# Performance work log

Measured on AMD Instinct MI355X. Metric: run time of the kernel, lower is better.

Reference implementation:

```python
import jax, jax.numpy as jnp
import numpy as np

BIN_ALPHA = 1.0  # alpha mixture factor from init
NEG_SLOPE = 0.1  # LeakyReLU slope


def setup_inputs() -> dict:
    key = jax.random.key(0)
    ks = jax.random.split(key, 10)
    B, N, BIN, D = 8, 19264, 100, 768
    gene_expression = jax.random.uniform(ks[0], (B, N), dtype=jnp.float32) * 10.0
    pad_mask = jax.random.randint(ks[1], (B, N), 0, 2, dtype=jnp.int32)
    masked_mask = jax.random.randint(ks[2], (B, N), 0, 2, dtype=jnp.int32)
    # layer1: Linear(1, BIN) -> weight (BIN,1) stored as (BIN,), bias (BIN,)
    w1 = jax.random.normal(ks[3], (BIN,), dtype=jnp.float32) * (1.0)
    b1 = jax.random.normal(ks[4], (BIN,), dtype=jnp.float32) * 0.1
    # layer2: Linear(BIN, BIN) -> weight (BIN,BIN), bias (BIN,)
    w2 = jax.random.normal(ks[5], (BIN, BIN), dtype=jnp.float32) * (1.0 / np.sqrt(BIN))
    b2 = jax.random.normal(ks[6], (BIN,), dtype=jnp.float32) * 0.1
    emb_table = jax.random.normal(ks[7], (BIN, D), dtype=jnp.float32)
    pad_emb = jax.random.normal(ks[8], (D,), dtype=jnp.float32)
    mask_emb = jax.random.normal(ks[9], (D,), dtype=jnp.float32)
    return {
        "gene_expression": gene_expression,
        "pad_mask": pad_mask,
        "masked_mask": masked_mask,
        "w1": w1, "b1": b1, "w2": w2, "b2": b2,
        "emb_table": emb_table, "pad_emb": pad_emb, "mask_emb": mask_emb,
    }


def reference(gene_expression, pad_mask, masked_mask, w1, b1, w2, b2,
              emb_table, pad_emb, mask_emb):
    # v1 = Linear(1, BIN): x[..., None] * w1 + b1 -> (B, N, BIN)
    v1 = gene_expression[..., None] * w1 + b1
    # LeakyReLU(0.1)
    v2 = jnp.where(v1 > 0, v1, NEG_SLOPE * v1)
    # cross-layer projection: v3 = alpha * v2 + Linear(BIN, BIN)(v2)
    v3 = BIN_ALPHA * v2 + jnp.einsum("bnk,jk->bnj", v2, w2) + b2
    weights = jax.nn.softmax(v3, axis=-1)          # (B, N, BIN)
    embeddings = jnp.einsum("bnk,kd->bnd", weights, emb_table)  # (B, N, D)
    # mixed_precision=True: pad/mask token embeddings are cast to bfloat16
    # before being scattered into the float32 output (then upcast on assign).
    pad_e = pad_emb.astype(jnp.bfloat16).astype(embeddings.dtype)
    mask_e = mask_emb.astype(jnp.bfloat16).astype(embeddings.dtype)
    embeddings = jnp.where((pad_mask != 0)[..., None], pad_e, embeddings)
    embeddings = jnp.where((masked_mask != 0)[..., None], mask_e, embeddings)
    return embeddings
```

## Files before the change

### kernel.cpp

```cpp
#include <hip/hip_runtime.h>
#include <hip/hip_bf16.h>

#define BINS 100
#define DIM 768
#define TPB 64
#define NTHREADS 256
#define KPAD 128
#define PITCH 136
#define NDT 12

#define OFF_ET   0
#define OFF_P    196608
#define OFF_Q    197120
#define OFF_TS   197632
#define OFF_KS   198144
#define OFF_R    198656
#define OFF_W2P  198720

typedef __attribute__((ext_vector_type(8))) short bf16x8;
typedef __attribute__((ext_vector_type(4))) float f32x4;

__device__ __forceinline__ unsigned short f2bf(float x) {
    __hip_bfloat16 h = __float2bfloat16(x);
    return *reinterpret_cast<unsigned short*>(&h);
}
__device__ __forceinline__ float bfrt(float x) {
    return __bfloat162float(__float2bfloat16(x));
}
__device__ __forceinline__ f32x4 bfrt4(f32x4 v) {
    f32x4 r;
    r.x = bfrt(v.x); r.y = bfrt(v.y); r.z = bfrt(v.z); r.w = bfrt(v.w);
    return r;
}

__global__ void prep(const float* __restrict__ emb,
                     const float* __restrict__ w1,
                     const float* __restrict__ b1,
                     const float* __restrict__ w2,
                     const float* __restrict__ b2,
                     unsigned char* __restrict__ ws)
{
    const int bid = blockIdx.x;
    const int tid = threadIdx.x;
    if (bid < DIM) {
        unsigned short* et = (unsigned short*)(ws + OFF_ET);
        float v = (tid < BINS) ? emb[(long)tid * DIM + bid] : 0.f;
        et[bid * KPAD + tid] = f2bf(v);
        return;
    }
    __shared__ float pl[BINS], ql[BINS], tl[BINS];
    float* Pv  = (float*)(ws + OFF_P);
    float* Qv  = (float*)(ws + OFF_Q);
    float* ts  = (float*)(ws + OFF_TS);
    int*   ks  = (int*)  (ws + OFF_KS);
    int*   Rp  = (int*)  (ws + OFF_R);
    float* w2p = (float*)(ws + OFF_W2P);
    if (tid < BINS) {
        float w = w1[tid], b = b1[tid];
        float f = (w > 0.f || (w == 0.f && b > 0.f)) ? 1.f : 0.1f;
        pl[tid] = w * f;
        ql[tid] = b * f;
        tl[tid] = (w != 0.f) ? (-b / w) : -1.f;
    }
    __syncthreads();
    if (tid < BINS) {
        const int j = tid;
        float P = pl[j];
        float Q = ql[j] + b2[j];
        for (int k = 0; k < BINS; k++) {
            float w = w2[j * BINS + k];
            P = fmaf(w, pl[k], P);
            Q = fmaf(w, ql[k], Q);
            w2p[j * BINS + k] = w + (j == k ? 1.f : 0.f);
        }
        Pv[j] = P; Qv[j] = Q;
        float tk = tl[j];
        int rank = 0;
        for (int k2 = 0; k2 < BINS; k2++) {
            float t2 = tl[k2];
            rank += (t2 > tk || (t2 == tk && k2 < j)) ? 1 : 0;
        }
        ts[rank] = tk;
        ks[rank] = j;
    }
    if (tid == 0) {
        int R = 0;
        for (int k = 0; k < BINS; k++) R += (tl[k] > 0.f) ? 1 : 0;
        *Rp = R;
    }
}

__global__ __launch_bounds__(NTHREADS, 8)
void ead_kernel(const float* __restrict__ gene,
                const int*   __restrict__ pad_mask,
                const int*   __restrict__ masked_mask,
                const float* __restrict__ w1,
                const float* __restrict__ b1,
                const unsigned short* __restrict__ et,
                const float* __restrict__ Pv,
                const float* __restrict__ Qv,
                const float* __restrict__ ts,
                const int*   __restrict__ ksod,
                const int*   __restrict__ Rp,
                const float* __restrict__ w2p,
                const float* __restrict__ pad_emb,
                const float* __restrict__ mask_emb,
                float* __restrict__ out,
                int T)
{
    __shared__ unsigned short wbf[TPB][PITCH];
    __shared__ float xs[TPB];
    __shared__ short surv[TPB];
    __shared__ short olist[TPB];
    __shared__ int Ssh, Osh;

    const int tid  = threadIdx.x;
    const int lane = tid & 63;
    const int wave = tid >> 6;
    const long t0  = (long)blockIdx.x * TPB;
    const int nvalid = min(TPB, (int)(T - t0));

    if (wave == 0) {
        int o = 3;
        if (lane < nvalid) {
            int pm  = pad_mask[t0 + lane];
            int msk = masked_mask[t0 + lane];
            o = msk ? 2 : (pm ? 1 : 0);
            xs[lane] = gene[t0 + lane];
        }
        unsigned long long bs = __ballot(o == 0);
        unsigned long long bo = __ballot(o == 1 || o == 2);
        int si = __popcll(bs & ((1ull << lane) - 1ull));
        int oi = __popcll(bo & ((1ull << lane) - 1ull));
        if (o == 0) surv[si] = (short)lane;
        if (o == 1 || o == 2) olist[oi] = (short)(lane | ((o == 2) ? 256 : 0));
        if (lane == 0) { Ssh = __popcll(bs); Osh = __popcll(bo); }
    }
    __syncthreads();
    const int S = Ssh, O = Osh;

    {
        const f32x4* pe = (const f32x4*)pad_emb;
        const f32x4* me = (const f32x4*)mask_emb;
        f32x4 p0 = bfrt4(pe[lane]), p1 = bfrt4(pe[lane + 64]), p2 = bfrt4(pe[lane + 128]);
        f32x4 m0 = bfrt4(me[lane]), m1 = bfrt4(me[lane + 64]), m2 = bfrt4(me[lane + 128]);
        for (int i = wave; i < O; i += 4) {
            int e = olist[i];
            int row = e & 63;
            bool mm = (e & 256) != 0;
            f32x4* orow = (f32x4*)(out + (t0 + row) * (long)DIM);
            __builtin_nontemporal_store(mm ? m0 : p0, orow + lane);
            __builtin_nontemporal_store(mm ? m1 : p1, orow + lane + 64);
            __builtin_nontemporal_store(mm ? m2 : p2, orow + lane + 128);
        }
    }

    {
        int s = wave + 4 * (lane >> 2);
        int part = lane & 3;
        const int j0 = part * 25;
        if (s < S) {
            float x = xs[surv[s]];
            float v3[25];
            #pragma unroll
            for (int i = 0; i < 25; i++)
                v3[i] = fmaf(x, Pv[j0 + i], Qv[j0 + i]);
            const int R = *Rp;
            for (int idx = 0; idx < R; ++idx) {
                float t = ts[idx];
                if (t <= x) break;
                int k = ksod[idx];
                float v1 = fmaf(x, w1[k], b1[k]);
                float d = 0.9f * fabsf(v1);
                const float* wc = w2p + j0 * BINS + k;
                #pragma unroll
                for (int i = 0; i < 25; i++)
                    v3[i] = fmaf(wc[i * BINS], d, v3[i]);
            }
            float vmax = -1e30f;
            #pragma unroll
            for (int i = 0; i < 25; i++) vmax = fmaxf(vmax, v3[i]);
            vmax = fmaxf(vmax, __shfl_xor(vmax, 1));
            vmax = fmaxf(vmax, __shfl_xor(vmax, 2));
            float sum = 0.f;
            #pragma unroll
            for (int i = 0; i < 25; i++) {
                v3[i] = __expf(v3[i] - vmax);
                sum += v3[i];
            }
            sum += __shfl_xor(sum, 1);
            sum += __shfl_xor(sum, 2);
            float inv = 1.f / sum;
            #pragma unroll
            for (int i = 0; i < 25; i++)
                wbf[s][j0 + i] = f2bf(v3[i] * inv);
            if (part == 3) {
                #pragma unroll
                for (int j = BINS; j < KPAD; j += 2)
                    *reinterpret_cast<unsigned int*>(&wbf[s][j]) = 0u;
            }
        }
    }
    __syncthreads();

    const int SM = (S + 15) >> 4;
    if (SM > 0) {
        const int arow = lane & 15;
        const int kgrp = lane >> 4;
        int tok0, tok1, tok2, tok3;
        {
            int sl;
            sl = 0 * 16 + arow; tok0 = (sl < S) ? surv[sl] : -1;
            sl = 1 * 16 + arow; tok1 = (SM > 1 && sl < S) ? surv[sl] : -1;
            sl = 2 * 16 + arow; tok2 = (SM > 2 && sl < S) ? surv[sl] : -1;
            sl = 3 * 16 + arow; tok3 = (SM > 3 && sl < S) ? surv[sl] : -1;
        }
        for (int c = 0; c < NDT; c++) {
            int dt = wave * 192 + c * 16;
            const unsigned short* ap = et + (long)(dt + arow) * KPAD + kgrp * 8;
            bf16x8 afr[4];
            #pragma unroll
            for (int kss = 0; kss < 4; kss++)
                afr[kss] = *(const bf16x8*)(ap + kss * 32);
            #pragma unroll
            for (int mt = 0; mt < 4; mt++) {
                if (mt < SM) {
                    f32x4 a = {0.f, 0.f, 0.f, 0.f};
                    #pragma unroll
                    for (int kss = 0; kss < 4; kss++) {
                        bf16x8 bfr = *(const bf16x8*)&wbf[mt * 16 + arow][kss * 32 + kgrp * 8];
                        a = __builtin_amdgcn_mfma_f32_16x16x32_bf16(afr[kss], bfr, a, 0, 0, 0);
                    }
                    int tkn = (mt == 0) ? tok0 : (mt == 1) ? tok1 : (mt == 2) ? tok2 : tok3;
                    if (tkn >= 0)
                        *(f32x4*)(out + (t0 + tkn) * (long)DIM + dt + kgrp * 4) = a;
                }
            }
        }
    }
}

extern "C" void kernel_launch(void* const* d_in, const int* in_sizes, int n_in,
                              void* d_out, int out_size, void* d_ws, size_t ws_size,
                              hipStream_t stream) {
    const float* gene  = (const float*)d_in[0];
    const int*   pm    = (const int*)  d_in[1];
    const int*   mm    = (const int*)  d_in[2];
    const float* w1    = (const float*)d_in[3];
    const float* b1    = (const float*)d_in[4];
    const float* w2    = (const float*)d_in[5];
    const float* b2    = (const float*)d_in[6];
    const float* emb   = (const float*)d_in[7];
    const float* pade  = (const float*)d_in[8];
    const float* maske = (const float*)d_in[9];
    float* out = (float*)d_out;
    unsigned char* ws = (unsigned char*)d_ws;

    int T = in_sizes[0];
    int nblk = (T + TPB - 1) / TPB;

    hipLaunchKernelGGL(prep, dim3(DIM + 1), dim3(KPAD), 0, stream,
                       emb, w1, b1, w2, b2, ws);
    hipLaunchKernelGGL(ead_kernel, dim3(nblk), dim3(NTHREADS), 0, stream,
                       gene, pm, mm, w1, b1,
                       (const unsigned short*)(ws + OFF_ET),
                       (const float*)(ws + OFF_P),
                       (const float*)(ws + OFF_Q),
                       (const float*)(ws + OFF_TS),
                       (const int*)(ws + OFF_KS),
                       (const int*)(ws + OFF_R),
                       (const float*)(ws + OFF_W2P),
                       pade, maske, out, T);
}
```

Baseline: 148.2 us.

## Restructure MFMA loop over token tiles, swizzle blocks, defer pad/mask stores

Result: slower. 197.1 us (+33.0%).

```diff
diff --git a/kernel.cpp b/kernel.cpp
--- a/kernel.cpp
+++ b/kernel.cpp
@@ -7,7 +7,6 @@
 #define NTHREADS 256
 #define KPAD 128
 #define PITCH 136
-#define NDT 12
 
 #define OFF_ET   0
 #define OFF_P    196608
@@ -90,7 +89,7 @@
     }
 }
 
-__global__ __launch_bounds__(NTHREADS, 8)
+__global__ __launch_bounds__(NTHREADS, 3)
 void ead_kernel(const float* __restrict__ gene,
                 const int*   __restrict__ pad_mask,
                 const int*   __restrict__ masked_mask,
@@ -112,12 +111,18 @@
     __shared__ float xs[TPB];
     __shared__ short surv[TPB];
     __shared__ short olist[TPB];
+    __shared__ f32x4 pes[192], mes[192];
     __shared__ int Ssh, Osh;
 
     const int tid  = threadIdx.x;
     const int lane = tid & 63;
     const int wave = tid >> 6;
-    const long t0  = (long)blockIdx.x * TPB;
+
+    const int nblk = (int)gridDim.x;
+    const int bid  = (int)blockIdx.x;
+    const int wg   = ((nblk & 7) == 0) ? ((bid & 7) * (nblk >> 3) + (bid >> 3))
+                                       : bid;
+    const long t0  = (long)wg * TPB;
     const int nvalid = min(TPB, (int)(T - t0));
 
     if (wave == 0) {
@@ -135,25 +140,13 @@
         if (o == 0) surv[si] = (short)lane;
         if (o == 1 || o == 2) olist[oi] = (short)(lane | ((o == 2) ? 256 : 0));
         if (lane == 0) { Ssh = __popcll(bs); Osh = __popcll(bo); }
+    } else {
+        int i = tid - 64;
+        pes[i] = bfrt4(((const f32x4*)pad_emb)[i]);
+        mes[i] = bfrt4(((const f32x4*)mask_emb)[i]);
     }
     __syncthreads();
     const int S = Ssh, O = Osh;
-
-    {
-        const f32x4* pe = (const f32x4*)pad_emb;
-        const f32x4* me = (const f32x4*)mask_emb;
-        f32x4 p0 = bfrt4(pe[lane]), p1 = bfrt4(pe[lane + 64]), p2 = bfrt4(pe[lane + 128]);
-        f32x4 m0 = bfrt4(me[lane]), m1 = bfrt4(me[lane + 64]), m2 = bfrt4(me[lane + 128]);
-        for (int i = wave; i < O; i += 4) {
-            int e = olist[i];
-            int row = e & 63;
-            bool mm = (e & 256) != 0;
-            f32x4* orow = (f32x4*)(out + (t0 + row) * (long)DIM);
-            __builtin_nontemporal_store(mm ? m0 : p0, orow + lane);
-            __builtin_nontemporal_store(mm ? m1 : p1, orow + lane + 64);
-            __builtin_nontemporal_store(mm ? m2 : p2, orow + lane + 128);
-        }
-    }
 
     {
         int s = wave + 4 * (lane >> 2);
@@ -204,38 +197,50 @@
     __syncthreads();
 
     const int SM = (S + 15) >> 4;
-    if (SM > 0) {
-        const int arow = lane & 15;
-        const int kgrp = lane >> 4;
-        int tok0, tok1, tok2, tok3;
-        {
-            int sl;
-            sl = 0 * 16 + arow; tok0 = (sl < S) ? surv[sl] : -1;
-            sl = 1 * 16 + arow; tok1 = (SM > 1 && sl < S) ? surv[sl] : -1;
-            sl = 2 * 16 + arow; tok2 = (SM > 2 && sl < S) ? surv[sl] : -1;
-            sl = 3 * 16 + arow; tok3 = (SM > 3 && sl < S) ? surv[sl] : -1;
-        }
-        for (int c = 0; c < NDT; c++) {
-            int dt = wave * 192 + c * 16;
-            const unsigned short* ap = et + (long)(dt + arow) * KPAD + kgrp * 8;
-            bf16x8 afr[4];
-            #pragma unroll
-            for (int kss = 0; kss < 4; kss++)
-                afr[kss] = *(const bf16x8*)(ap + kss * 32);
-            #pragma unroll
-            for (int mt = 0; mt < 4; mt++) {
-                if (mt < SM) {
-                    f32x4 a = {0.f, 0.f, 0.f, 0.f};
-                    #pragma unroll
-                    for (int kss = 0; kss < 4; kss++) {
-                        bf16x8 bfr = *(const bf16x8*)&wbf[mt * 16 + arow][kss * 32 + kgrp * 8];
-                        a = __builtin_amdgcn_mfma_f32_16x16x32_bf16(afr[kss], bfr, a, 0, 0, 0);
-                    }
-                    int tkn = (mt == 0) ? tok0 : (mt == 1) ? tok1 : (mt == 2) ? tok2 : tok3;
-                    if (tkn >= 0)
-                        *(f32x4*)(out + (t0 + tkn) * (long)DIM + dt + kgrp * 4) = a;
-                }
-            }
+    const int arow = lane & 15;
+    const int kgrp = lane >> 4;
+    const int dbase = wave * 192;
+    for (int mt = 0; mt < SM; mt++) {
+        int sl = mt * 16 + arow;
+        int tkn = (sl < S) ? surv[sl] : -1;
+        bf16x8 bfr0 = *(const bf16x8*)&wbf[mt * 16 + arow][0  + kgrp * 8];
+        bf16x8 bfr1 = *(const bf16x8*)&wbf[mt * 16 + arow][32 + kgrp * 8];
+        bf16x8 bfr2 = *(const bf16x8*)&wbf[mt * 16 + arow][64 + kgrp * 8];
+        bf16x8 bfr3 = *(const bf16x8*)&wbf[mt * 16 + arow][96 + kgrp * 8];
+        f32x4 acc[12];
+        #pragma unroll
+        for (int c = 0; c < 12; c++) {
+            const unsigned short* ap = et + (long)(dbase + c * 16 + arow) * KPAD + kgrp * 8;
+            bf16x8 a0 = *(const bf16x8*)(ap);
+            bf16x8 a1 = *(const bf16x8*)(ap + 32);
+            bf16x8 a2 = *(const bf16x8*)(ap + 64);
+            bf16x8 a3 = *(const bf16x8*)(ap + 96);
+            f32x4 t = {0.f, 0.f, 0.f, 0.f};
+            t = __builtin_amdgcn_mfma_f32_16x16x32_bf16(a0, bfr0, t, 0, 0, 0);
+            t = __builtin_amdgcn_mfma_f32_16x16x32_bf16(a1, bfr1, t, 0, 0, 0);
+            t = __builtin_amdgcn_mfma_f32_16x16x32_bf16(a2, bfr2, t, 0, 0, 0);
+            t = __builtin_amdgcn_mfma_f32_16x16x32_bf16(a3, bfr3, t, 0, 0, 0);
+            acc[c] = t;
+        }
+        if (tkn >= 0) {
+            float* orow = out + (t0 + tkn) * (long)DIM + dbase + kgrp * 4;
+            #pragma unroll
+            for (int c = 0; c < 12; c++)
+                *(f32x4*)(orow + c * 16) = acc[c];
+        }
+    }
+
+    if (O > 0) {
+        f32x4 p0 = pes[lane], p1 = pes[lane + 64], p2 = pes[lane + 128];
+        f32x4 m0 = mes[lane], m1 = mes[lane + 64], m2 = mes[lane + 128];
+        for (int i = wave; i < O; i += 4) {
+            int e = olist[i];
+            int row = e & 63;
+            bool mm = (e & 256) != 0;
+            f32x4* orow = (f32x4*)(out + (t0 + row) * (long)DIM);
+            __builtin_nontemporal_store(mm ? m0 : p0, orow + lane);
+            __builtin_nontemporal_store(mm ? m1 : p1, orow + lane + 64);
+            __builtin_nontemporal_store(mm ? m2 : p2, orow + lane + 128);
         }
     }
 }
```

## Split pad/mask row fill into dedicated blocks separate from survivor compute blocks

Applied to the files above, without the earlier changes.

Result: slower. 179.9 us (+21.4%).

```diff
diff --git a/kernel.cpp b/kernel.cpp
--- a/kernel.cpp
+++ b/kernel.cpp
@@ -7,7 +7,7 @@
 #define NTHREADS 256
 #define KPAD 128
 #define PITCH 136
-#define NDT 12
+#define ROWS_OV 256
 
 #define OFF_ET   0
 #define OFF_P    196608
@@ -106,54 +106,62 @@
                 const float* __restrict__ pad_emb,
                 const float* __restrict__ mask_emb,
                 float* __restrict__ out,
-                int T)
+                int nov, int T)
 {
     __shared__ unsigned short wbf[TPB][PITCH];
     __shared__ float xs[TPB];
     __shared__ short surv[TPB];
-    __shared__ short olist[TPB];
-    __shared__ int Ssh, Osh;
+    __shared__ int Ssh;
 
     const int tid  = threadIdx.x;
     const int lane = tid & 63;
     const int wave = tid >> 6;
-    const long t0  = (long)blockIdx.x * TPB;
-    const int nvalid = min(TPB, (int)(T - t0));
-
-    if (wave == 0) {
-        int o = 3;
-        if (lane < nvalid) {
-            int pm  = pad_mask[t0 + lane];
-            int msk = masked_mask[t0 + lane];
-            o = msk ? 2 : (pm ? 1 : 0);
-            xs[lane] = gene[t0 + lane];
-        }
-        unsigned long long bs = __ballot(o == 0);
-        unsigned long long bo = __ballot(o == 1 || o == 2);
-        int si = __popcll(bs & ((1ull << lane) - 1ull));
-        int oi = __popcll(bo & ((1ull << lane) - 1ull));
-        if (o == 0) surv[si] = (short)lane;
-        if (o == 1 || o == 2) olist[oi] = (short)(lane | ((o == 2) ? 256 : 0));
-        if (lane == 0) { Ssh = __popcll(bs); Osh = __popcll(bo); }
-    }
-    __syncthreads();
-    const int S = Ssh, O = Osh;
-
-    {
+
+    if ((int)blockIdx.x < nov) {
+        const long r0 = (long)blockIdx.x * ROWS_OV + wave * 64;
+        int pmv = 0, mmv = 0;
+        if (r0 + lane < T) {
+            pmv = pad_mask[r0 + lane];
+            mmv = masked_mask[r0 + lane];
+        }
         const f32x4* pe = (const f32x4*)pad_emb;
         const f32x4* me = (const f32x4*)mask_emb;
         f32x4 p0 = bfrt4(pe[lane]), p1 = bfrt4(pe[lane + 64]), p2 = bfrt4(pe[lane + 128]);
         f32x4 m0 = bfrt4(me[lane]), m1 = bfrt4(me[lane + 64]), m2 = bfrt4(me[lane + 128]);
-        for (int i = wave; i < O; i += 4) {
-            int e = olist[i];
-            int row = e & 63;
-            bool mm = (e & 256) != 0;
-            f32x4* orow = (f32x4*)(out + (t0 + row) * (long)DIM);
-            __builtin_nontemporal_store(mm ? m0 : p0, orow + lane);
-            __builtin_nontemporal_store(mm ? m1 : p1, orow + lane + 64);
-            __builtin_nontemporal_store(mm ? m2 : p2, orow + lane + 128);
-        }
-    }
+        const long rend = min((long)T, r0 + 64);
+        for (long r = r0; r < rend; r++) {
+            int i = (int)(r - r0);
+            int pm = __shfl(pmv, i);
+            int mm = __shfl(mmv, i);
+            if (mm | pm) {
+                f32x4* orow = (f32x4*)(out + r * (long)DIM);
+                orow[lane]       = mm ? m0 : p0;
+                orow[lane + 64]  = mm ? m1 : p1;
+                orow[lane + 128] = mm ? m2 : p2;
+            }
+        }
+        return;
+    }
+
+    const long t0 = (long)(blockIdx.x - nov) * TPB;
+    const int nvalid = min(TPB, (int)(T - t0));
+
+    if (wave == 0) {
+        int o = 1;
+        if (lane < nvalid) {
+            int pm  = pad_mask[t0 + lane];
+            int msk = masked_mask[t0 + lane];
+            o = (msk || pm) ? 1 : 0;
+            xs[lane] = gene[t0 + lane];
+        }
+        unsigned long long bs = __ballot(o == 0);
+        int si = __popcll(bs & ((1ull << lane) - 1ull));
+        if (o == 0) surv[si] = (short)lane;
+        if (lane == 0) Ssh = __popcll(bs);
+    }
+    __syncthreads();
+    const int S = Ssh;
+    if (S == 0) return;
 
     {
         int s = wave + 4 * (lane >> 2);
@@ -204,37 +212,36 @@
     __syncthreads();
 
     const int SM = (S + 15) >> 4;
-    if (SM > 0) {
-        const int arow = lane & 15;
-        const int kgrp = lane >> 4;
-        int tok0, tok1, tok2, tok3;
-        {
-            int sl;
-            sl = 0 * 16 + arow; tok0 = (sl < S) ? surv[sl] : -1;
-            sl = 1 * 16 + arow; tok1 = (SM > 1 && sl < S) ? surv[sl] : -1;
-            sl = 2 * 16 + arow; tok2 = (SM > 2 && sl < S) ? surv[sl] : -1;
-            sl = 3 * 16 + arow; tok3 = (SM > 3 && sl < S) ? surv[sl] : -1;
-        }
-        for (int c = 0; c < NDT; c++) {
-            int dt = wave * 192 + c * 16;
-            const unsigned short* ap = et + (long)(dt + arow) * KPAD + kgrp * 8;
-            bf16x8 afr[4];
-            #pragma unroll
-            for (int kss = 0; kss < 4; kss++)
-                afr[kss] = *(const bf16x8*)(ap + kss * 32);
-            #pragma unroll
-            for (int mt = 0; mt < 4; mt++) {
-                if (mt < SM) {
-                    f32x4 a = {0.f, 0.f, 0.f, 0.f};
-                    #pragma unroll
-                    for (int kss = 0; kss < 4; kss++) {
-                        bf16x8 bfr = *(const bf16x8*)&wbf[mt * 16 + arow][kss * 32 + kgrp * 8];
-                        a = __builtin_amdgcn_mfma_f32_16x16x32_bf16(afr[kss], bfr, a, 0, 0, 0);
-                    }
-                    int tkn = (mt == 0) ? tok0 : (mt == 1) ? tok1 : (mt == 2) ? tok2 : tok3;
-                    if (tkn >= 0)
-                        *(f32x4*)(out + (t0 + tkn) * (long)DIM + dt + kgrp * 4) = a;
+    const int arow = lane & 15;
+    const int kgrp = lane >> 4;
+    const int dbase = wave * 192;
+    int tok0, tok1, tok2, tok3;
+    {
+        int sl;
+        sl = 0 * 16 + arow; tok0 = (sl < S) ? surv[sl] : -1;
+        sl = 1 * 16 + arow; tok1 = (SM > 1 && sl < S) ? surv[sl] : -1;
+        sl = 2 * 16 + arow; tok2 = (SM > 2 && sl < S) ? surv[sl] : -1;
+        sl = 3 * 16 + arow; tok3 = (SM > 3 && sl < S) ? surv[sl] : -1;
+    }
+    for (int c = 0; c < 12; c++) {
+        int dt = dbase + c * 16;
+        const unsigned short* ap = et + (long)(dt + arow) * KPAD + kgrp * 8;
+        bf16x8 afr[4];
+        #pragma unroll
+        for (int kss = 0; kss < 4; kss++)
+            afr[kss] = *(const bf16x8*)(ap + kss * 32);
+        #pragma unroll
+        for (int mt = 0; mt < 4; mt++) {
+            if (mt < SM) {
+                f32x4 a = {0.f, 0.f, 0.f, 0.f};
+                #pragma unroll
+                for (int kss = 0; kss < 4; kss++) {
+                    bf16x8 bfr = *(const bf16x8*)&wbf[mt * 16 + arow][kss * 32 + kgrp * 8];
+                    a = __builtin_amdgcn_mfma_f32_16x16x32_bf16(afr[kss], bfr, a, 0, 0, 0);
                 }
+                int tkn = (mt == 0) ? tok0 : (mt == 1) ? tok1 : (mt == 2) ? tok2 : tok3;
+                if (tkn >= 0)
+                    *(f32x4*)(out + (t0 + tkn) * (long)DIM + dt + kgrp * 4) = a;
             }
         }
     }
@@ -257,11 +264,12 @@
     unsigned char* ws = (unsigned char*)d_ws;
 
     int T = in_sizes[0];
-    int nblk = (T + TPB - 1) / TPB;
+    int nov = (T + ROWS_OV - 1) / ROWS_OV;
+    int nsv = (T + TPB - 1) / TPB;
 
     hipLaunchKernelGGL(prep, dim3(DIM + 1), dim3(KPAD), 0, stream,
                        emb, w1, b1, w2, b2, ws);
-    hipLaunchKernelGGL(ead_kernel, dim3(nblk), dim3(NTHREADS), 0, stream,
+    hipLaunchKernelGGL(ead_kernel, dim3(nov + nsv), dim3(NTHREADS), 0, stream,
                        gene, pm, mm, w1, b1,
                        (const unsigned short*)(ws + OFF_ET),
                        (const float*)(ws + OFF_P),
@@ -270,5 +278,5 @@
                        (const int*)(ws + OFF_KS),
                        (const int*)(ws + OFF_R),
                        (const float*)(ws + OFF_W2P),
-                       pade, maske, out, T);
-}
+                       pade, maske, out, nov, T);
+}
```
